# Kernel optimization log

Measured on AMD Instinct MI355X. Metric: run time of the kernel, lower is better.

## Reference

```python
import jax, jax.numpy as jnp
import numpy as np
import math

B, C, H, W = 4, 128, 180, 180
CCAM, HEADS, DH, N = 256, 4, 32, 20000
HD = HEADS * DH
GAMMA = 0.08
EPS = 1e-6


def setup_inputs() -> dict:
    key = jax.random.key(0)
    ks = jax.random.split(key, 10)
    return {
        "lidar_bev": jax.random.normal(ks[0], (B, C, H, W), jnp.float32),
        "cam_bev_tokens": jax.random.normal(ks[1], (B, N, CCAM), jnp.float32),
        "gate_weights": jax.random.uniform(ks[2], (B, N), jnp.float32),
        "range_alpha": jax.random.uniform(ks[3], (1, 1, H, W), jnp.float32),
        # q_proj: Conv2d(C, HD, 1) -> weight [HD, C] (1x1 conv == per-pixel linear), bias [HD]
        "q_w": jax.random.normal(ks[4], (HD, C), jnp.float32) * 0.02,
        "q_bias": jax.random.normal(ks[5], (HD,), jnp.float32) * 0.02,
        # k/v_proj: Linear(CCAM, HD, bias=False)
        "k_w": jax.random.normal(ks[6], (HD, CCAM), jnp.float32) * 0.02,
        "v_w": jax.random.normal(ks[7], (HD, CCAM), jnp.float32) * 0.02,
        # out: Conv2d(HD, C, 1, bias=False) -> W_out [C, HD]
        "out_w": jax.random.normal(ks[8], (C, HD), jnp.float32) * 0.02,
        "cam_bev_indices": jax.random.randint(ks[9], (B, N, 2), 0, H, jnp.int32),
    }


def reference(lidar_bev, cam_bev_tokens, gate_weights, range_alpha,
              q_w, q_bias, k_w, v_w, out_w, cam_bev_indices):
    scale = 1.0 / math.sqrt(DH)
    # 1x1 conv q projection -> [B, h, d, H*W]
    q = jnp.einsum('bchw,oc->bohw', lidar_bev, q_w) + q_bias[None, :, None, None]
    q = q.reshape(B, HEADS, DH, H * W)

    i = jnp.clip(cam_bev_indices[..., 0], 0, H - 1)
    j = jnp.clip(cam_bev_indices[..., 1], 0, W - 1)
    lin = i * W + j  # [B, N]

    # gather q at sparse BEV locations -> [B, h, d, N]
    q_g = jnp.take_along_axis(q, lin[:, None, None, :], axis=3)

    # k/v projections -> [B, h, d, N]
    k = jnp.einsum('bnc,oc->bno', cam_bev_tokens, k_w).reshape(B, N, HEADS, DH).transpose(0, 2, 3, 1)
    v = jnp.einsum('bnc,oc->bno', cam_bev_tokens, v_w).reshape(B, N, HEADS, DH).transpose(0, 2, 3, 1)

    # elementwise-multiply attention: logits [B, h, N], softmax over the N tokens
    attn = jax.nn.softmax((q_g * k).sum(axis=2) * scale, axis=-1) * gate_weights[:, None, :]
    fused = (attn[:, :, None, :] * v).reshape(B, HD, N)  # [B, h*d, N]
    out_tok = jnp.einsum('co,bon->bcn', out_w, fused)    # [B, C, N]

    # per-batch scatter (index_add) + hit counts (bincount)
    def scatter_b(tok, lin_b):
        df = jnp.zeros((C, H * W), tok.dtype).at[:, lin_b].add(tok)
        hits = jnp.zeros((H * W,), tok.dtype).at[lin_b].add(1.0)
        return df, hits

    delta_flat, hits = jax.vmap(scatter_b)(out_tok, lin)  # [B,C,HW], [B,HW]
    mask = (hits > 0).astype(lidar_bev.dtype)  # [B, HW]

    # mean over hit locations (per batch, per channel), subtract on hits only
    mean_on = (delta_flat * mask[:, None, :]).sum(axis=-1, keepdims=True) \
              / (mask.sum(axis=-1)[:, None, None] + EPS)  # [B, C, 1]
    tmp = (delta_flat - mean_on * mask[:, None, :]).reshape(B, C, H, W)
    tmp = tmp * range_alpha * GAMMA
    return lidar_bev + tmp
```

## Files before the change

kernel.cpp:

```cpp
#include <hip/hip_runtime.h>

#define BB 4
#define CC 128
#define HH 180
#define WWW 180
#define HWHW (HH*WWW)
#define CCAMD 256
#define NHEADS 4
#define HDD 128
#define NT 20000
#define MTOT 80000
#define GAMMA_C 0.08f
#define EPS_C 1e-6f
#define SCALE_C 0.17677669529663687f

typedef short bf16x8 __attribute__((ext_vector_type(8)));
typedef float f32x4 __attribute__((ext_vector_type(4)));

typedef __attribute__((address_space(1))) const unsigned int GU;
typedef __attribute__((address_space(3))) unsigned int LU;

static __device__ __forceinline__ void gll16(const void* g, void* l) {
  __builtin_amdgcn_global_load_lds((GU*)g, (LU*)l, 16, 0, 0);
}

#define WAIT_VMCNT0() asm volatile("s_waitcnt vmcnt(0)" ::: "memory")
#define WAIT_VMCNT2() asm volatile("s_waitcnt vmcnt(2)" ::: "memory")
#define WAIT_VMCNT3() asm volatile("s_waitcnt vmcnt(3)" ::: "memory")
#define WAIT_LGKM0()  asm volatile("s_waitcnt lgkmcnt(0)" ::: "memory")

static __device__ __forceinline__ unsigned short f2bf(float x) {
  unsigned int b = __float_as_uint(x);
  unsigned int r = (b + 0x7fffu + ((b >> 16) & 1u)) >> 16;
  return (unsigned short)r;
}
static __device__ __forceinline__ float b2f(unsigned short u) {
  return __uint_as_float(((unsigned int)u) << 16);
}

static __device__ __forceinline__ float warpMax(float v) {
#pragma unroll
  for (int o = 32; o >= 1; o >>= 1) v = fmaxf(v, __shfl_xor(v, o));
  return v;
}
static __device__ __forceinline__ float warpSum(float v) {
#pragma unroll
  for (int o = 32; o >= 1; o >>= 1) v += __shfl_xor(v, o);
  return v;
}
static __device__ __forceinline__ int warpSumI(int v) {
#pragma unroll
  for (int o = 32; o >= 1; o >>= 1) v += __shfl_xor(v, o);
  return v;
}

__global__ __launch_bounds__(256) void k_prep_pix(
    const float* __restrict__ kw, const float* __restrict__ vw,
    const float* __restrict__ qw, const float* __restrict__ ow,
    unsigned short* __restrict__ kvw, unsigned short* __restrict__ qwb,
    unsigned short* __restrict__ owb, const int* __restrict__ cidx,
    int* __restrict__ pix_ws, int* __restrict__ cnt_pix)
{
  if (blockIdx.x < 96) {
    const int t = blockIdx.x * 256 + threadIdx.x;
    float4 f;
    unsigned short* dst;
    if (t < 16384) {
      f = (t < 8192) ? ((const float4*)kw)[t] : ((const float4*)vw)[t - 8192];
      dst = kvw + (size_t)t * 4;
    } else if (t < 20480) {
      const int i = t - 16384;
      f = ((const float4*)qw)[i];
      dst = qwb + (size_t)i * 4;
    } else {
      const int i = t - 20480;
      f = ((const float4*)ow)[i];
      dst = owb + (size_t)i * 4;
    }
    ushort4 u;
    u.x = f2bf(f.x); u.y = f2bf(f.y); u.z = f2bf(f.z); u.w = f2bf(f.w);
    *(ushort4*)dst = u;
  } else {
    const int t = (blockIdx.x - 96) * 256 + threadIdx.x;
    if (t >= MTOT) return;
    const int2 ij = *(const int2*)(cidx + (size_t)t * 2);
    int ii = ij.x; ii = ii < 0 ? 0 : (ii > HH - 1 ? HH - 1 : ii);
    int jj = ij.y; jj = jj < 0 ? 0 : (jj > WWW - 1 ? WWW - 1 : jj);
    const int pix = ii * WWW + jj;
    pix_ws[t] = pix;
    atomicAdd(cnt_pix + (size_t)(t / NT) * HWHW + pix, 1);
  }
}

__global__ __launch_bounds__(256) void k_tr2(
    const float* __restrict__ lidar, unsigned short* __restrict__ lidar_t)
{
  const int b = blockIdx.y;
  const int p = blockIdx.x * 256 + threadIdx.x;
  if (p >= HWHW) return;
  const int z = blockIdx.z;
  const float* src = lidar + ((size_t)b * CC + z * 64) * HWHW + p;
  unsigned short* dst = lidar_t + ((size_t)b * HWHW + p) * 128 + z * 64;
#pragma unroll
  for (int c8 = 0; c8 < 8; ++c8) {
    bf16x8 v;
#pragma unroll
    for (int e = 0; e < 8; ++e)
      v[e] = (short)f2bf(src[(size_t)(c8 * 8 + e) * HWHW]);
    ((bf16x8*)dst)[c8] = v;
  }
}

__global__ __launch_bounds__(256) void k_scanA(
    const int* __restrict__ cnt, int* __restrict__ bsum)
{
  const int b = blockIdx.y, blk = blockIdx.x;
  const int idx = blk * 256 + threadIdx.x;
  int v = (idx < HWHW) ? cnt[(size_t)b * HWHW + idx] : 0;
  v = warpSumI(v);
  __shared__ int ws[4];
  const int wave = threadIdx.x >> 6, lane = threadIdx.x & 63;
  if (lane == 0) ws[wave] = v;
  __syncthreads();
  if (threadIdx.x == 0)
    bsum[b * 128 + blk] = ws[0] + ws[1] + ws[2] + ws[3];
}

__global__ __launch_bounds__(128) void k_scanB(
    const int* __restrict__ bsum, int* __restrict__ boff)
{
  __shared__ int s[128];
  const int b = blockIdx.x, t = threadIdx.x;
  s[t] = bsum[b * 128 + t];
  __syncthreads();
#pragma unroll
  for (int off = 1; off < 128; off <<= 1) {
    int v = (t >= off) ? s[t - off] : 0;
    __syncthreads();
    s[t] += v;
    __syncthreads();
  }
  boff[b * 128 + t] = (t == 0) ? 0 : s[t - 1];
}

__global__ __launch_bounds__(256) void k_scanC(
    const int* __restrict__ cnt, const int* __restrict__ boff,
    int* __restrict__ start)
{
  const int b = blockIdx.y, blk = blockIdx.x;
  const int idx = blk * 256 + threadIdx.x;
  const int wave = threadIdx.x >> 6, lane = threadIdx.x & 63;
  int v = (idx < HWHW) ? cnt[(size_t)b * HWHW + idx] : 0;
  int inc = v;
#pragma unroll
  for (int off = 1; off < 64; off <<= 1) {
    int u = __shfl_up(inc, off, 64);
    if (lane >= off) inc += u;
  }
  __shared__ int ws[4];
  if (lane == 63) ws[wave] = inc;
  __syncthreads();
  int wo = 0;
#pragma unroll
  for (int w = 0; w < 4; ++w)
    if (w < wave) wo += ws[w];
  if (idx < HWHW)
    start[(size_t)b * HWHW + idx] = boff[b * 128 + blk] + wo + inc - v;
}

__global__ __launch_bounds__(256) void k_reorder(
    const int* __restrict__ pix_ws, const int* __restrict__ start,
    int* __restrict__ fill, int* __restrict__ sortn)
{
  const int t = blockIdx.x * 256 + threadIdx.x;
  if (t >= MTOT) return;
  const int b = t / NT, n = t - b * NT;
  const int pix = pix_ws[t];
  const int pos = atomicAdd(fill + (size_t)b * HWHW + pix, 1);
  sortn[(size_t)b * NT + start[(size_t)b * HWHW + pix] + pos] = n;
}

template<int KSTEPS, int KW, int AMODE, int EPI, int NOUT>
__global__ __launch_bounds__(512) void k_pipe(
    const float* __restrict__ Af32, const unsigned short* __restrict__ Abf,
    const unsigned short* __restrict__ Bw, const float* __restrict__ bias,
    unsigned short* __restrict__ Dbf, const int* __restrict__ pixw,
    float* __restrict__ aux,
    const unsigned short* __restrict__ kvb, float* __restrict__ meanr,
    const float* __restrict__ smMp, const float* __restrict__ smSinvp,
    const float* __restrict__ gatep, const float* __restrict__ logp,
    const int* __restrict__ sortn)
{
  __shared__ unsigned short lds[24576];
  const int tid = threadIdx.x;
  const int lane = tid & 63, wave = tid >> 6;
  const int wm = wave >> 2, wn = wave & 3;
  const int l16 = lane & 15, kg = lane >> 4;
  const int mblk = blockIdx.x, nblk = blockIdx.y;
  const int sr_rd = (l16 >> 1) & 3;

  const int row_s = wave * 16 + (lane >> 2);
  const int chunk_s = lane & 3;
  const int swz_s = chunk_s ^ ((lane >> 3) & 3);
  const int a_dst = row_s * 32 + swz_s * 8;

  const unsigned short* bsrc = Bw + (size_t)(nblk * 128 + row_s) * KW + swz_s * 8;

  const float* asrc_f32 = nullptr;
  const unsigned short* asrc_bf = nullptr;
  float coef4[4] = {0.f, 0.f, 0.f, 0.f};
  if constexpr (AMODE == 0) {
    asrc_f32 = Af32 + (size_t)(mblk * 128 + row_s) * KW + chunk_s * 8;
  } else if constexpr (AMODE == 2) {
    const int r = mblk * 128 + row_s;
    const int bb = r / NT;
    asrc_bf = Abf + ((size_t)bb * HWHW + pixw[r]) * 128 + swz_s * 8;
  } else {
    const int r = mblk * 128 + row_s;
    const int bb = r / NT, pos = r - bb * NT;
    const int n = sortn[(size_t)bb * NT + pos];
    asrc_bf = Abf + ((size_t)bb * NT + n) * 256 + 128 + chunk_s * 8;
    const float ga = gatep[(size_t)bb * NT + n];
#pragma unroll
    for (int h = 0; h < 4; ++h) {
      const int bh = bb * NHEADS + h;
      coef4[h] = __expf(logp[(size_t)bh * NT + n] - smMp[bh]) * smSinvp[bh] * ga;
    }
  }

  f32x4 acc[4][2];
#pragma unroll
  for (int i = 0; i < 4; ++i)
#pragma unroll
    for (int j = 0; j < 2; ++j) acc[i][j] = (f32x4)0.0f;

  float4 afx[2], afy[2];
  bf16x8 av[2];

  auto issueA = [&](int kt, int s, int buf) {
    if constexpr (AMODE == 0) {
      afx[s] = *(const float4*)(asrc_f32 + kt * 32);
      afy[s] = *(const float4*)(asrc_f32 + kt * 32 + 4);
    } else if constexpr (AMODE == 2) {
      gll16(asrc_bf + kt * 32, &lds[buf * 8192 + wave * 512]);
    } else {
      av[s] = *(const bf16x8*)(asrc_bf + kt * 32);
    }
  };
  auto issueB = [&](int kt, int buf) {
    gll16(bsrc + kt * 32, &lds[buf * 8192 + 4096 + wave * 512]);
  };
  auto writeA = [&](int kt, int s, int buf) {
    bf16x8 v;
    if constexpr (AMODE == 0) {
      v[0] = (short)f2bf(afx[s].x); v[1] = (short)f2bf(afx[s].y);
      v[2] = (short)f2bf(afx[s].z); v[3] = (short)f2bf(afx[s].w);
      v[4] = (short)f2bf(afy[s].x); v[5] = (short)f2bf(afy[s].y);
      v[6] = (short)f2bf(afy[s].z); v[7] = (short)f2bf(afy[s].w);
    } else {
      const float c = coef4[kt];
#pragma unroll
      for (int e = 0; e < 8; ++e)
        v[e] = (short)f2bf(b2f((unsigned short)av[s][e]) * c);
    }
    *(bf16x8*)&lds[buf * 8192 + a_dst] = v;
  };
  auto compute = [&](int buf) {
    const int base = buf * 8192;
    bf16x8 a[4], b[2];
#pragma unroll
    for (int mf = 0; mf < 4; ++mf) {
      const int row = wm * 64 + mf * 16 + l16;
      a[mf] = *(const bf16x8*)&lds[base + row * 32 + ((kg ^ sr_rd) << 3)];
    }
#pragma unroll
    for (int nf = 0; nf < 2; ++nf) {
      const int row = wn * 32 + nf * 16 + l16;
      b[nf] = *(const bf16x8*)&lds[base + 4096 + row * 32 + ((kg ^ sr_rd) << 3)];
    }
#pragma unroll
    for (int mf = 0; mf < 4; ++mf)
#pragma unroll
      for (int nf = 0; nf < 2; ++nf)
        acc[mf][nf] =
            __builtin_amdgcn_mfma_f32_16x16x32_bf16(a[mf], b[nf], acc[mf][nf], 0, 0, 0);
  };

  issueA(0, 0, 0); issueB(0, 0);
  issueA(1, 1, 1); issueB(1, 1);
  if constexpr (AMODE != 2) writeA(0, 0, 0);

#pragma unroll
  for (int t = 0; t < KSTEPS; ++t) {
    if (t < KSTEPS - 1) {
      if constexpr (AMODE == 0) WAIT_VMCNT3(); else WAIT_VMCNT2();
    } else {
      WAIT_VMCNT0();
    }
    WAIT_LGKM0();
    __builtin_amdgcn_s_barrier();
    __builtin_amdgcn_sched_barrier(0);
    if (t + 2 < KSTEPS) {
      issueA(t + 2, t & 1, (t + 2) % 3);
      issueB(t + 2, (t + 2) % 3);
    }
    compute(t % 3);
    if constexpr (AMODE != 2) {
      if (t + 1 < KSTEPS) writeA(t + 1, (t + 1) & 1, (t + 1) % 3);
    }
  }
  __syncthreads();

  float* scratch = (float*)lds;

  if constexpr (EPI == 0) {
#pragma unroll
    for (int mf = 0; mf < 4; ++mf) {
#pragma unroll
      for (int j = 0; j < 4; ++j) {
        const int row = mblk * 128 + wm * 64 + mf * 16 + kg * 4 + j;
        unsigned short* dr = Dbf + (size_t)row * NOUT + nblk * 128 + wn * 32 + l16;
#pragma unroll
        for (int nf = 0; nf < 2; ++nf)
          dr[nf * 16] = f2bf(acc[mf][nf][j]);
      }
    }
  } else if constexpr (EPI == 2) {
    float bv[2];
#pragma unroll
    for (int nf = 0; nf < 2; ++nf)
      bv[nf] = bias[wn * 32 + nf * 16 + l16];
#pragma unroll
    for (int mf = 0; mf < 4; ++mf) {
#pragma unroll
      for (int j = 0; j < 4; ++j) {
        const int rl = wm * 64 + mf * 16 + kg * 4 + j;
        const int row = mblk * 128 + rl;
        const unsigned short* kr = kvb + (size_t)row * 256 + wn * 32 + l16;
        float s = (acc[mf][0][j] + bv[0]) * b2f(kr[0]) +
                  (acc[mf][1][j] + bv[1]) * b2f(kr[16]);
        s += __shfl_xor(s, 8, 16); s += __shfl_xor(s, 4, 16);
        s += __shfl_xor(s, 2, 16); s += __shfl_xor(s, 1, 16);
        if (l16 == 0) scratch[rl * 4 + wn] = s;
      }
    }
    __syncthreads();
    if (tid < 128) {
      const int row = mblk * 128 + tid;
      const int bb = row / NT, n = row - bb * NT;
#pragma unroll
      for (int h = 0; h < 4; ++h)
        aux[((size_t)bb * NHEADS + h) * NT + n] = scratch[tid * 4 + h] * SCALE_C;
    }
  } else {
    if (tid < 256) scratch[tid] = 0.0f;
    __syncthreads();
    const int b0 = (mblk * 128) / NT;
#pragma unroll
    for (int mf = 0; mf < 4; ++mf) {
      const int baser = mblk * 128 + wm * 64 + mf * 16 + kg * 4;
      const int bb = baser / NT;
      const int bsel = (bb != b0) ? 1 : 0;
      float s[2] = {0.0f, 0.0f};
#pragma unroll
      for (int j = 0; j < 4; ++j) {
        const int row = baser + j;
        unsigned short* dr = Dbf + (size_t)row * 128 + wn * 32 + l16;
#pragma unroll
        for (int nf = 0; nf < 2; ++nf) {
          dr[nf * 16] = f2bf(acc[mf][nf][j]);
          s[nf] += acc[mf][nf][j];
        }
      }
#pragma unroll
      for (int nf = 0; nf < 2; ++nf)
        atomicAdd(&scratch[bsel * 128 + wn * 32 + nf * 16 + l16], s[nf]);
    }
    __syncthreads();
    const int b1 = (mblk * 128 + 127) / NT;
    if (tid < 128) atomicAdd(meanr + (size_t)b0 * 128 + tid, scratch[tid]);
    else if (tid < 256 && b1 != b0)
      atomicAdd(meanr + (size_t)b1 * 128 + (tid - 128), scratch[tid]);
  }
}

__global__ __launch_bounds__(256) void k_smpart(
    const float* __restrict__ logits, float* __restrict__ pm,
    float* __restrict__ ps)
{
  const int ch = blockIdx.x, bh = blockIdx.y;
  const float* L = logits + (size_t)bh * NT + ch * 2500;
  const int tid = threadIdx.x;
  __shared__ float sred[4];

  float m = -INFINITY;
  for (int i = tid; i < 2500; i += 256) m = fmaxf(m, L[i]);
  m = warpMax(m);
  if ((tid & 63) == 0) sred[tid >> 6] = m;
  __syncthreads();
  m = fmaxf(fmaxf(sred[0], sred[1]), fmaxf(sred[2], sred[3]));

  float s = 0.0f;
  for (int i = tid; i < 2500; i += 256) s += __expf(L[i] - m);
  s = warpSum(s);
  __syncthreads();
  if ((tid & 63) == 0) sred[tid >> 6] = s;
  __syncthreads();
  if (tid == 0) {
    pm[bh * 8 + ch] = m;
    ps[bh * 8 + ch] = sred[0] + sred[1] + sred[2] + sred[3];
  }
}

__global__ __launch_bounds__(256) void k_cntfix(
    const int* __restrict__ cnt_pix, float* __restrict__ cntB,
    const float* __restrict__ pm, const float* __restrict__ ps,
    float* __restrict__ smM, float* __restrict__ smSinv)
{
  const int b = blockIdx.x;
  const int tid = threadIdx.x;
  float s = 0.0f;
  for (int i = tid; i < HWHW; i += 256)
    s += (cnt_pix[(size_t)b * HWHW + i] > 0) ? 1.0f : 0.0f;
  s = warpSum(s);
  __shared__ float sred[4];
  if ((tid & 63) == 0) sred[tid >> 6] = s;
  __syncthreads();
  if (tid == 0) cntB[b] = sred[0] + sred[1] + sred[2] + sred[3];
  if (b == 0 && tid < BB * NHEADS) {
    float M = -INFINITY;
#pragma unroll
    for (int c = 0; c < 8; ++c) M = fmaxf(M, pm[tid * 8 + c]);
    float S = 0.0f;
#pragma unroll
    for (int c = 0; c < 8; ++c) S += ps[tid * 8 + c] * __expf(pm[tid * 8 + c] - M);
    smM[tid] = M;
    smSinv[tid] = 1.0f / S;
  }
}

__global__ __launch_bounds__(512) void k_final2(
    const float* __restrict__ lidar, const float* __restrict__ alpha,
    const int* __restrict__ cnt_pix, const int* __restrict__ start,
    const unsigned short* __restrict__ out_tok,
    const float* __restrict__ mean_raw, const float* __restrict__ cntB,
    float* __restrict__ out)
{
  __shared__ float tile[80 * 136];
  const int b = blockIdx.y;
  const int p0 = blockIdx.x * 80;
  const int t = threadIdx.x;

  const int g = t >> 5, l32 = t & 31;
#pragma unroll
  for (int i = 0; i < 5; ++i) {
    const int pl = i * 16 + g;
    const int p = p0 + pl;
    const int st = start[(size_t)b * HWHW + p];
    const int cn = cnt_pix[(size_t)b * HWHW + p];
    float4 a = make_float4(0.0f, 0.0f, 0.0f, 0.0f);
    const unsigned short* rp = out_tok + ((size_t)b * NT + st) * 128 + l32 * 4;
    for (int k = 0; k < cn; ++k) {
      const ushort4 u = *(const ushort4*)(rp + (size_t)k * 128);
      a.x += b2f(u.x); a.y += b2f(u.y); a.z += b2f(u.z); a.w += b2f(u.w);
    }
    *(float4*)&tile[pl * 136 + ((l32 ^ (pl & 7)) << 2)] = a;
  }
  __syncthreads();

  const int c = t >> 2, sub = t & 3;
  const int cq = c >> 2, cr = c & 3;
  const float mn = mean_raw[b * 128 + c] / (cntB[b] + EPS_C);
  const size_t cbase = ((size_t)b * CC + c) * HWHW + p0;
  const int* cnb = cnt_pix + (size_t)b * HWHW + p0;
#pragma unroll
  for (int j = 0; j < 5; ++j) {
    const int pq = j * 16 + sub * 4;
    float4 d;
    d.x = tile[(pq + 0) * 136 + (((cq ^ ((pq + 0) & 7)) << 2) | cr)];
    d.y = tile[(pq + 1) * 136 + (((cq ^ ((pq + 1) & 7)) << 2) | cr)];
    d.z = tile[(pq + 2) * 136 + (((cq ^ ((pq + 2) & 7)) << 2) | cr)];
    d.w = tile[(pq + 3) * 136 + (((cq ^ ((pq + 3) & 7)) << 2) | cr)];
    const float4 li = *(const float4*)(lidar + cbase + pq);
    const float4 al = *(const float4*)(alpha + p0 + pq);
    const int4 hc = *(const int4*)(cnb + pq);
    float4 o;
    o.x = li.x + (d.x - (hc.x > 0 ? mn : 0.0f)) * al.x * GAMMA_C;
    o.y = li.y + (d.y - (hc.y > 0 ? mn : 0.0f)) * al.y * GAMMA_C;
    o.z = li.z + (d.z - (hc.z > 0 ? mn : 0.0f)) * al.z * GAMMA_C;
    o.w = li.w + (d.w - (hc.w > 0 ? mn : 0.0f)) * al.w * GAMMA_C;
    *(float4*)(out + cbase + pq) = o;
  }
}

extern "C" void kernel_launch(void* const* d_in, const int* in_sizes, int n_in,
                              void* d_out, int out_size, void* d_ws, size_t ws_size,
                              hipStream_t stream)
{
  const float* lidar  = (const float*)d_in[0];
  const float* tokens = (const float*)d_in[1];
  const float* gate   = (const float*)d_in[2];
  const float* alpha  = (const float*)d_in[3];
  const float* q_w    = (const float*)d_in[4];
  const float* q_b    = (const float*)d_in[5];
  const float* k_w    = (const float*)d_in[6];
  const float* v_w    = (const float*)d_in[7];
  const float* out_w  = (const float*)d_in[8];
  const int*   cidx   = (const int*)d_in[9];
  float* out = (float*)d_out;

  char* W = (char*)d_ws;
  unsigned short* kv_bf   = (unsigned short*)(W + 0);
  unsigned short* lidar_t = (unsigned short*)(W + 40960000);
  unsigned short* out_tok = (unsigned short*)(W + 74137600);
  float* logits  = (float*)(W + 94617600);
  int*   pix_ws  = (int*)(W + 95897600);
  int*   sortn   = (int*)(W + 96217600);
  int*   cnt_pix = (int*)(W + 96537600);
  int*   start   = (int*)(W + 97056000);
  int*   fill    = (int*)(W + 97574400);
  float* mean_raw = (float*)(W + 98092800);
  float* cntB     = (float*)(W + 98094848);
  unsigned short* kvw_bf = (unsigned short*)(W + 98094912);
  unsigned short* qw_bf  = (unsigned short*)(W + 98225984);
  unsigned short* ow_bf  = (unsigned short*)(W + 98258752);
  float* pm     = (float*)(W + 98291520);
  float* ps     = (float*)(W + 98292032);
  float* smM    = (float*)(W + 98292544);
  float* smSinv = (float*)(W + 98292608);
  int*   bsum   = (int*)(W + 98292672);
  int*   boff   = (int*)(W + 98294720);

  hipMemsetAsync(cnt_pix, 0, (size_t)BB * HWHW * sizeof(int), stream);
  hipMemsetAsync(fill, 0, (size_t)BB * HWHW * sizeof(int), stream);
  hipMemsetAsync(mean_raw, 0, 2048 + 64, stream);

  k_prep_pix<<<dim3(409), 256, 0, stream>>>(k_w, v_w, q_w, out_w, kvw_bf,
                                            qw_bf, ow_bf, cidx, pix_ws, cnt_pix);
  k_tr2<<<dim3(127, BB, 2), 256, 0, stream>>>(lidar, lidar_t);
  k_scanA<<<dim3(128, BB), 256, 0, stream>>>(cnt_pix, bsum);
  k_scanB<<<dim3(BB), 128, 0, stream>>>(bsum, boff);
  k_scanC<<<dim3(128, BB), 256, 0, stream>>>(cnt_pix, boff, start);
  k_reorder<<<dim3(313), 256, 0, stream>>>(pix_ws, start, fill, sortn);
  k_pipe<8, 256, 0, 0, 256><<<dim3(625, 2), 512, 0, stream>>>(
      tokens, nullptr, kvw_bf, nullptr, kv_bf, nullptr, nullptr, nullptr,
      nullptr, nullptr, nullptr, nullptr, nullptr, nullptr);
  k_pipe<4, 128, 2, 2, 128><<<dim3(625, 1), 512, 0, stream>>>(
      nullptr, lidar_t, qw_bf, q_b, nullptr, pix_ws, logits, kv_bf,
      nullptr, nullptr, nullptr, nullptr, nullptr, nullptr);
  k_smpart<<<dim3(8, BB * NHEADS), 256, 0, stream>>>(logits, pm, ps);
  k_cntfix<<<dim3(BB), 256, 0, stream>>>(cnt_pix, cntB, pm, ps, smM, smSinv);
  k_pipe<4, 128, 4, 3, 128><<<dim3(625, 1), 512, 0, stream>>>(
      nullptr, kv_bf, ow_bf, nullptr, out_tok, nullptr, nullptr, nullptr,
      mean_raw, smM, smSinv, gate, logits, sortn);
  k_final2<<<dim3(405, BB), 512, 0, stream>>>(lidar, alpha, cnt_pix, start,
                                              out_tok, mean_raw, cntB, out);
}
```

Measured before the change: 217.3 us.

## Merge independent stages into fewer launches via block-index dispatch

Folds the lidar transpose, the first scan pass and the KV projection GEMM into one launch. The second scan pass is folded in with the Q/logits GEMM, and the softmax partials with the token reorder, each split by block index. The scan is reorganized to 64 blocks of 512 per batch, so the middle pass becomes a single-wave shuffle scan. This cuts kernel launches and gaps between dependent stages and lets independent work share the GPU. The cost is heterogeneous blocks whose register and LDS use is set by the heaviest branch, which may hurt occupancy for the light branches.

```diff
diff --git a/kernel.cpp b/kernel.cpp
--- a/kernel.cpp
+++ b/kernel.cpp
@@ -92,111 +92,21 @@
   }
 }
 
-__global__ __launch_bounds__(256) void k_tr2(
-    const float* __restrict__ lidar, unsigned short* __restrict__ lidar_t)
-{
-  const int b = blockIdx.y;
-  const int p = blockIdx.x * 256 + threadIdx.x;
-  if (p >= HWHW) return;
-  const int z = blockIdx.z;
-  const float* src = lidar + ((size_t)b * CC + z * 64) * HWHW + p;
-  unsigned short* dst = lidar_t + ((size_t)b * HWHW + p) * 128 + z * 64;
-#pragma unroll
-  for (int c8 = 0; c8 < 8; ++c8) {
-    bf16x8 v;
-#pragma unroll
-    for (int e = 0; e < 8; ++e)
-      v[e] = (short)f2bf(src[(size_t)(c8 * 8 + e) * HWHW]);
-    ((bf16x8*)dst)[c8] = v;
-  }
-}
-
-__global__ __launch_bounds__(256) void k_scanA(
-    const int* __restrict__ cnt, int* __restrict__ bsum)
-{
-  const int b = blockIdx.y, blk = blockIdx.x;
-  const int idx = blk * 256 + threadIdx.x;
-  int v = (idx < HWHW) ? cnt[(size_t)b * HWHW + idx] : 0;
-  v = warpSumI(v);
-  __shared__ int ws[4];
-  const int wave = threadIdx.x >> 6, lane = threadIdx.x & 63;
-  if (lane == 0) ws[wave] = v;
-  __syncthreads();
-  if (threadIdx.x == 0)
-    bsum[b * 128 + blk] = ws[0] + ws[1] + ws[2] + ws[3];
-}
-
-__global__ __launch_bounds__(128) void k_scanB(
-    const int* __restrict__ bsum, int* __restrict__ boff)
-{
-  __shared__ int s[128];
-  const int b = blockIdx.x, t = threadIdx.x;
-  s[t] = bsum[b * 128 + t];
-  __syncthreads();
-#pragma unroll
-  for (int off = 1; off < 128; off <<= 1) {
-    int v = (t >= off) ? s[t - off] : 0;
-    __syncthreads();
-    s[t] += v;
-    __syncthreads();
-  }
-  boff[b * 128 + t] = (t == 0) ? 0 : s[t - 1];
-}
-
-__global__ __launch_bounds__(256) void k_scanC(
-    const int* __restrict__ cnt, const int* __restrict__ boff,
-    int* __restrict__ start)
-{
-  const int b = blockIdx.y, blk = blockIdx.x;
-  const int idx = blk * 256 + threadIdx.x;
-  const int wave = threadIdx.x >> 6, lane = threadIdx.x & 63;
-  int v = (idx < HWHW) ? cnt[(size_t)b * HWHW + idx] : 0;
-  int inc = v;
-#pragma unroll
-  for (int off = 1; off < 64; off <<= 1) {
-    int u = __shfl_up(inc, off, 64);
-    if (lane >= off) inc += u;
-  }
-  __shared__ int ws[4];
-  if (lane == 63) ws[wave] = inc;
-  __syncthreads();
-  int wo = 0;
-#pragma unroll
-  for (int w = 0; w < 4; ++w)
-    if (w < wave) wo += ws[w];
-  if (idx < HWHW)
-    start[(size_t)b * HWHW + idx] = boff[b * 128 + blk] + wo + inc - v;
-}
-
-__global__ __launch_bounds__(256) void k_reorder(
-    const int* __restrict__ pix_ws, const int* __restrict__ start,
-    int* __restrict__ fill, int* __restrict__ sortn)
-{
-  const int t = blockIdx.x * 256 + threadIdx.x;
-  if (t >= MTOT) return;
-  const int b = t / NT, n = t - b * NT;
-  const int pix = pix_ws[t];
-  const int pos = atomicAdd(fill + (size_t)b * HWHW + pix, 1);
-  sortn[(size_t)b * NT + start[(size_t)b * HWHW + pix] + pos] = n;
-}
-
 template<int KSTEPS, int KW, int AMODE, int EPI, int NOUT>
-__global__ __launch_bounds__(512) void k_pipe(
+static __device__ void pipe_body(
+    int mblk, int nblk, unsigned short* lds,
     const float* __restrict__ Af32, const unsigned short* __restrict__ Abf,
     const unsigned short* __restrict__ Bw, const float* __restrict__ bias,
     unsigned short* __restrict__ Dbf, const int* __restrict__ pixw,
-    float* __restrict__ aux,
-    const unsigned short* __restrict__ kvb, float* __restrict__ meanr,
-    const float* __restrict__ smMp, const float* __restrict__ smSinvp,
-    const float* __restrict__ gatep, const float* __restrict__ logp,
-    const int* __restrict__ sortn)
-{
-  __shared__ unsigned short lds[24576];
+    float* __restrict__ aux, const unsigned short* __restrict__ kvb,
+    float* __restrict__ meanr, const float* __restrict__ smMp,
+    const float* __restrict__ smSinvp, const float* __restrict__ gatep,
+    const float* __restrict__ logp, const int* __restrict__ sortn)
+{
   const int tid = threadIdx.x;
   const int lane = tid & 63, wave = tid >> 6;
   const int wm = wave >> 2, wn = wave & 3;
   const int l16 = lane & 15, kg = lane >> 4;
-  const int mblk = blockIdx.x, nblk = blockIdx.y;
   const int sr_rd = (l16 >> 1) & 3;
 
   const int row_s = wave * 16 + (lane >> 2);
@@ -384,31 +294,140 @@
   }
 }
 
-__global__ __launch_bounds__(256) void k_smpart(
+__global__ __launch_bounds__(512) void k_m1(
+    const float* __restrict__ lidar, unsigned short* __restrict__ lidar_t,
+    const int* __restrict__ cnt_pix, int* __restrict__ bsum,
+    const float* __restrict__ tokens, const unsigned short* __restrict__ kvw,
+    unsigned short* __restrict__ kv_bf)
+{
+  __shared__ unsigned short lds[24576];
+  const int bid = blockIdx.x;
+  if (bid < 254) {
+    const int idx = bid * 512 + threadIdx.x;
+    if (idx >= BB * HWHW) return;
+    const int b = idx / HWHW, p = idx - b * HWHW;
+    const float* src = lidar + (size_t)b * CC * HWHW + p;
+    unsigned short* dst = lidar_t + (size_t)idx * 128;
+#pragma unroll
+    for (int c8 = 0; c8 < 16; ++c8) {
+      bf16x8 v;
+#pragma unroll
+      for (int e = 0; e < 8; ++e)
+        v[e] = (short)f2bf(src[(size_t)(c8 * 8 + e) * HWHW]);
+      ((bf16x8*)dst)[c8] = v;
+    }
+  } else if (bid < 510) {
+    __shared__ int ws[8];
+    const int s = bid - 254;
+    const int b = s >> 6, blk = s & 63;
+    const int idx = blk * 512 + threadIdx.x;
+    int v = (idx < HWHW) ? cnt_pix[(size_t)b * HWHW + idx] : 0;
+    v = warpSumI(v);
+    const int wave = threadIdx.x >> 6, lane = threadIdx.x & 63;
+    if (lane == 0) ws[wave] = v;
+    __syncthreads();
+    if (threadIdx.x == 0) {
+      int s8 = 0;
+#pragma unroll
+      for (int w = 0; w < 8; ++w) s8 += ws[w];
+      bsum[b * 64 + blk] = s8;
+    }
+  } else {
+    const int g = bid - 510;
+    pipe_body<8, 256, 0, 0, 256>(g % 625, g / 625, lds, tokens, nullptr,
+                                 kvw, nullptr, kv_bf, nullptr, nullptr,
+                                 nullptr, nullptr, nullptr, nullptr,
+                                 nullptr, nullptr, nullptr);
+  }
+}
+
+__global__ __launch_bounds__(64) void k_scanB(
+    const int* __restrict__ bsum, int* __restrict__ boff)
+{
+  const int b = blockIdx.x, t = threadIdx.x;
+  const int v = bsum[b * 64 + t];
+  int inc = v;
+#pragma unroll
+  for (int off = 1; off < 64; off <<= 1) {
+    int u = __shfl_up(inc, off, 64);
+    if (t >= off) inc += u;
+  }
+  boff[b * 64 + t] = inc - v;
+}
+
+__global__ __launch_bounds__(512) void k_m2(
+    const int* __restrict__ cnt_pix, const int* __restrict__ boff,
+    int* __restrict__ start, const unsigned short* __restrict__ lidar_t,
+    const unsigned short* __restrict__ qwb, const float* __restrict__ qb,
+    const int* __restrict__ pixw, float* __restrict__ logits,
+    const unsigned short* __restrict__ kv_bf)
+{
+  __shared__ unsigned short lds[24576];
+  const int bid = blockIdx.x;
+  if (bid < 256) {
+    __shared__ int ws[8];
+    const int b = bid >> 6, blk = bid & 63;
+    const int idx = blk * 512 + threadIdx.x;
+    const int wave = threadIdx.x >> 6, lane = threadIdx.x & 63;
+    int v = (idx < HWHW) ? cnt_pix[(size_t)b * HWHW + idx] : 0;
+    int inc = v;
+#pragma unroll
+    for (int off = 1; off < 64; off <<= 1) {
+      int u = __shfl_up(inc, off, 64);
+      if (lane >= off) inc += u;
+    }
+    if (lane == 63) ws[wave] = inc;
+    __syncthreads();
+    int wo = 0;
+#pragma unroll
+    for (int w = 0; w < 8; ++w)
+      if (w < wave) wo += ws[w];
+    if (idx < HWHW)
+      start[(size_t)b * HWHW + idx] = boff[b * 64 + blk] + wo + inc - v;
+  } else {
+    pipe_body<4, 128, 2, 2, 128>(bid - 256, 0, lds, nullptr, lidar_t, qwb,
+                                 qb, nullptr, pixw, logits, kv_bf, nullptr,
+                                 nullptr, nullptr, nullptr, nullptr, nullptr);
+  }
+}
+
+__global__ __launch_bounds__(256) void k_m3(
     const float* __restrict__ logits, float* __restrict__ pm,
-    float* __restrict__ ps)
-{
-  const int ch = blockIdx.x, bh = blockIdx.y;
-  const float* L = logits + (size_t)bh * NT + ch * 2500;
-  const int tid = threadIdx.x;
-  __shared__ float sred[4];
-
-  float m = -INFINITY;
-  for (int i = tid; i < 2500; i += 256) m = fmaxf(m, L[i]);
-  m = warpMax(m);
-  if ((tid & 63) == 0) sred[tid >> 6] = m;
-  __syncthreads();
-  m = fmaxf(fmaxf(sred[0], sred[1]), fmaxf(sred[2], sred[3]));
-
-  float s = 0.0f;
-  for (int i = tid; i < 2500; i += 256) s += __expf(L[i] - m);
-  s = warpSum(s);
-  __syncthreads();
-  if ((tid & 63) == 0) sred[tid >> 6] = s;
-  __syncthreads();
-  if (tid == 0) {
-    pm[bh * 8 + ch] = m;
-    ps[bh * 8 + ch] = sred[0] + sred[1] + sred[2] + sred[3];
+    float* __restrict__ ps, const int* __restrict__ pix_ws,
+    const int* __restrict__ start, int* __restrict__ fill,
+    int* __restrict__ sortn)
+{
+  const int bid = blockIdx.x;
+  if (bid < 128) {
+    const int ch = bid & 7, bh = bid >> 3;
+    const float* L = logits + (size_t)bh * NT + ch * 2500;
+    const int tid = threadIdx.x;
+    __shared__ float sred[4];
+
+    float m = -INFINITY;
+    for (int i = tid; i < 2500; i += 256) m = fmaxf(m, L[i]);
+    m = warpMax(m);
+    if ((tid & 63) == 0) sred[tid >> 6] = m;
+    __syncthreads();
+    m = fmaxf(fmaxf(sred[0], sred[1]), fmaxf(sred[2], sred[3]));
+
+    float s = 0.0f;
+    for (int i = tid; i < 2500; i += 256) s += __expf(L[i] - m);
+    s = warpSum(s);
+    __syncthreads();
+    if ((tid & 63) == 0) sred[tid >> 6] = s;
+    __syncthreads();
+    if (tid == 0) {
+      pm[bh * 8 + ch] = m;
+      ps[bh * 8 + ch] = sred[0] + sred[1] + sred[2] + sred[3];
+    }
+  } else {
+    const int t = (bid - 128) * 256 + threadIdx.x;
+    if (t >= MTOT) return;
+    const int b = t / NT, n = t - b * NT;
+    const int pix = pix_ws[t];
+    const int pos = atomicAdd(fill + (size_t)b * HWHW + pix, 1);
+    sortn[(size_t)b * NT + start[(size_t)b * HWHW + pix] + pos] = n;
   }
 }
 
@@ -437,6 +456,19 @@
     smM[tid] = M;
     smSinv[tid] = 1.0f / S;
   }
+}
+
+__global__ __launch_bounds__(512) void k_out(
+    const unsigned short* __restrict__ kv_bf, const unsigned short* __restrict__ owb,
+    unsigned short* __restrict__ out_tok, float* __restrict__ meanr,
+    const float* __restrict__ smM, const float* __restrict__ smSinv,
+    const float* __restrict__ gate, const float* __restrict__ logits,
+    const int* __restrict__ sortn)
+{
+  __shared__ unsigned short lds[24576];
+  pipe_body<4, 128, 4, 3, 128>(blockIdx.x, 0, lds, nullptr, kv_bf, owb,
+                               nullptr, out_tok, nullptr, nullptr, nullptr,
+                               meanr, smM, smSinv, gate, logits, sortn);
 }
 
 __global__ __launch_bounds__(512) void k_final2(
@@ -529,7 +561,7 @@
   float* smM    = (float*)(W + 98292544);
   float* smSinv = (float*)(W + 98292608);
   int*   bsum   = (int*)(W + 98292672);
-  int*   boff   = (int*)(W + 98294720);
+  int*   boff   = (int*)(W + 98293696);
 
   hipMemsetAsync(cnt_pix, 0, (size_t)BB * HWHW * sizeof(int), stream);
   hipMemsetAsync(fill, 0, (size_t)BB * HWHW * sizeof(int), stream);
@@ -537,22 +569,15 @@
 
   k_prep_pix<<<dim3(409), 256, 0, stream>>>(k_w, v_w, q_w, out_w, kvw_bf,
                                             qw_bf, ow_bf, cidx, pix_ws, cnt_pix);
-  k_tr2<<<dim3(127, BB, 2), 256, 0, stream>>>(lidar, lidar_t);
-  k_scanA<<<dim3(128, BB), 256, 0, stream>>>(cnt_pix, bsum);
-  k_scanB<<<dim3(BB), 128, 0, stream>>>(bsum, boff);
-  k_scanC<<<dim3(128, BB), 256, 0, stream>>>(cnt_pix, boff, start);
-  k_reorder<<<dim3(313), 256, 0, stream>>>(pix_ws, start, fill, sortn);
-  k_pipe<8, 256, 0, 0, 256><<<dim3(625, 2), 512, 0, stream>>>(
-      tokens, nullptr, kvw_bf, nullptr, kv_bf, nullptr, nullptr, nullptr,
-      nullptr, nullptr, nullptr, nullptr, nullptr, nullptr);
-  k_pipe<4, 128, 2, 2, 128><<<dim3(625, 1), 512, 0, stream>>>(
-      nullptr, lidar_t, qw_bf, q_b, nullptr, pix_ws, logits, kv_bf,
-      nullptr, nullptr, nullptr, nullptr, nullptr, nullptr);
-  k_smpart<<<dim3(8, BB * NHEADS), 256, 0, stream>>>(logits, pm, ps);
+  k_m1<<<dim3(1760), 512, 0, stream>>>(lidar, lidar_t, cnt_pix, bsum,
+                                       tokens, kvw_bf, kv_bf);
+  k_scanB<<<dim3(BB), 64, 0, stream>>>(bsum, boff);
+  k_m2<<<dim3(881), 512, 0, stream>>>(cnt_pix, boff, start, lidar_t, qw_bf,
+                                      q_b, pix_ws, logits, kv_bf);
+  k_m3<<<dim3(441), 256, 0, stream>>>(logits, pm, ps, pix_ws, start, fill, sortn);
   k_cntfix<<<dim3(BB), 256, 0, stream>>>(cnt_pix, cntB, pm, ps, smM, smSinv);
-  k_pipe<4, 128, 4, 3, 128><<<dim3(625, 1), 512, 0, stream>>>(
-      nullptr, kv_bf, ow_bf, nullptr, out_tok, nullptr, nullptr, nullptr,
-      mean_raw, smM, smSinv, gate, logits, sortn);
+  k_out<<<dim3(625), 512, 0, stream>>>(kv_bf, ow_bf, out_tok, mean_raw,
+                                       smM, smSinv, gate, logits, sortn);
   k_final2<<<dim3(405, BB), 512, 0, stream>>>(lidar, alpha, cnt_pix, start,
                                               out_tok, mean_raw, cntB, out);
 }
```

Measured after the change: 208.4 us. -4.1%, faster.
